# Optimization experiments

Measured on AMD Instinct MI355X. Metric: run time of the kernel, lower is better.

The kernel has to match this reference:

```python
import jax, jax.numpy as jnp
import numpy as np

GRID = 32
N_NODES = GRID * GRID          # 1024
PATCH = 1
C_IN = 3
NODE_F = C_IN * PATCH * PATCH  # 3
HID = 256
N_CLASSES = 10


def _build_norm_adj():
    # 5-point grid stencil + self loops, symmetrically normalized: D^-1/2 A D^-1/2
    adj = np.zeros((N_NODES, N_NODES), dtype=np.float32)
    idx = np.arange(N_NODES)
    i, j = idx // GRID, idx % GRID
    adj[idx, idx] = 1.0
    for di, dj in [(-1, 0), (1, 0), (0, -1), (0, 1)]:
        ni, nj = i + di, j + dj
        ok = (ni >= 0) & (ni < GRID) & (nj >= 0) & (nj < GRID)
        adj[idx[ok], (ni * GRID + nj)[ok]] = 1.0
    deg = adj.sum(axis=1)
    dis = np.where(deg > 0, deg ** -0.5, 0.0).astype(np.float32)
    return jnp.asarray(dis[:, None] * adj * dis[None, :])


def _image_to_graph(x):
    # [B,C,H,W] -> [B, grid, patch, grid, patch] blocks -> [B, N, C*patch^2]
    B = x.shape[0]
    x = x.reshape(B, C_IN, GRID, PATCH, GRID, PATCH)
    x = jnp.transpose(x, (0, 2, 4, 1, 3, 5))
    return x.reshape(B, N_NODES, NODE_F)


def setup_inputs() -> dict:
    key = jax.random.key(0)
    ks = jax.random.split(key, 10)
    s = 0.05
    return {
        "x": jax.random.normal(ks[0], (256, 3, 32, 32), dtype=jnp.float32),
        "W1": jax.random.normal(ks[1], (HID, NODE_F), dtype=jnp.float32) * s,
        "b1": jnp.zeros((HID,), dtype=jnp.float32),
        "W2": jax.random.normal(ks[2], (HID, HID), dtype=jnp.float32) * s,
        "b2": jnp.zeros((HID,), dtype=jnp.float32),
        "W3": jax.random.normal(ks[3], (HID // 2, HID), dtype=jnp.float32) * s,
        "b3": jnp.zeros((HID // 2,), dtype=jnp.float32),
        "Wc": jax.random.normal(ks[4], (N_CLASSES, N_NODES * (HID // 2)), dtype=jnp.float32) * s,
        "bc": jnp.zeros((N_CLASSES,), dtype=jnp.float32),
        "adj": _build_norm_adj(),
    }


def _gc(h, W, b, adj):
    # Linear, then fixed-adjacency aggregation, then ReLU
    h = jnp.einsum('bnf,hf->bnh', h, W) + b
    h = jnp.einsum('mn,bnh->bmh', adj, h)
    return jax.nn.relu(h)


def reference(x, W1, b1, W2, b2, W3, b3, Wc, bc, adj):
    h = _image_to_graph(x)                 # [B, N, 3]
    h = _gc(h, W1, b1, adj)                # [B, N, 256]
    h = _gc(h, W2, b2, adj)                # [B, N, 256]
    h = _gc(h, W3, b3, adj)                # [B, N, 128]
    h = h.reshape(h.shape[0], -1)          # [B, N*128]
    return h @ Wc.T + bc                   # [B, 10]
```

## Files before the change

### kernel.cpp

```cpp
#include <hip/hip_runtime.h>
#include <stdint.h>

#define N_NODES 1024
#define NCLS 10
#define KDIM 131072

typedef unsigned short u16;
typedef __bf16 bf16x8 __attribute__((ext_vector_type(8)));
typedef float f32x4 __attribute__((ext_vector_type(4)));
typedef float f32x2 __attribute__((ext_vector_type(2)));

__device__ __forceinline__ float b2f_lo(uint32_t u) {
  union { float f; uint32_t u; } v; v.u = u << 16; return v.f;
}
__device__ __forceinline__ float b2f_hi(uint32_t u) {
  union { float f; uint32_t u; } v; v.u = u & 0xFFFF0000u; return v.f;
}
__device__ __forceinline__ u16 f2b(float f) {
  union { float f; uint32_t u; } v; v.f = f;
  uint32_t r = v.u + 0x7FFF + ((v.u >> 16) & 1);
  return (u16)(r >> 16);
}
__device__ __forceinline__ uint32_t pkbf(float a, float b) {
#if __has_builtin(__builtin_amdgcn_cvt_pk_bf16_f32)
  typedef __bf16 bf2 __attribute__((ext_vector_type(2)));
  bf2 r = __builtin_amdgcn_cvt_pk_bf16_f32(a, b);
  union { bf2 v; uint32_t u; } c; c.v = r; return c.u;
#else
  union { float f; uint32_t u; } va, vb; va.f = a; vb.f = b;
  uint32_t ra = (va.u + 0x7FFF + ((va.u >> 16) & 1)) >> 16;
  uint32_t rb = (vb.u + 0x7FFF + ((vb.u >> 16) & 1)) & 0xFFFF0000u;
  return ra | rb;
#endif
}
__device__ __forceinline__ uint32_t pkbf2(f32x2 z) { return pkbf(z.x, z.y); }

__device__ __forceinline__ void async_copy16(const u16* g, u16* l) {
  __builtin_amdgcn_global_load_lds(
      (const __attribute__((address_space(1))) void*)g,
      (__attribute__((address_space(3))) void*)l, 16, 0, 0);
}

__device__ __forceinline__ void agg8p(uint4 v, float c, f32x2* acc) {
  const uint32_t* u = (const uint32_t*)&v;
  f32x2 cv = {c, c};
#pragma unroll
  for (int e = 0; e < 4; e++) {
    f32x2 p = {b2f_lo(u[e]), b2f_hi(u[e])};
    acc[e] += p * cv;
  }
}

__global__ __launch_bounds__(256) void prep_wfrag_kernel(const float* __restrict__ w,
                                                         u16* __restrict__ o, int n) {
  int i = blockIdx.x * 256 + threadIdx.x;
  if (i >= n) return;
  int j = i & 7;
  int l = (i >> 3) & 63;
  int kq = (i >> 9) & 7;
  int nt = i >> 12;
  o[i] = f2b(w[(nt * 16 + (l & 15)) * 256 + kq * 32 + (l >> 4) * 8 + j]);
}

__global__ __launch_bounds__(256) void prep_wc_kernel(const float* __restrict__ wc,
                                                      u16* __restrict__ o) {
  int i = blockIdx.x * 256 + threadIdx.x;
  int row = i >> 17;
  int col = i & (KDIM - 1);
  o[i] = (row < NCLS) ? f2b(wc[row * KDIM + col]) : (u16)0;
}

__global__ __launch_bounds__(256) void prep_tab_kernel(const float* __restrict__ adj,
                                                       int* __restrict__ nbi,
                                                       float* __restrict__ nbc,
                                                       float* __restrict__ r) {
  int m = blockIdx.x * 256 + threadIdx.x;
  if (m >= N_NODES) return;
  int i = m >> 5, j = m & 31;
  const float* arow = adj + (size_t)m * N_NODES;
  int n[5]; float c[5];
  n[0] = m;                      c[0] = arow[m];
  n[1] = (i > 0)  ? m - 32 : m;  c[1] = (i > 0)  ? arow[m - 32] : 0.f;
  n[2] = (i < 31) ? m + 32 : m;  c[2] = (i < 31) ? arow[m + 32] : 0.f;
  n[3] = (j > 0)  ? m - 1  : m;  c[3] = (j > 0)  ? arow[m - 1]  : 0.f;
  n[4] = (j < 31) ? m + 1  : m;  c[4] = (j < 31) ? arow[m + 1]  : 0.f;
  float s = 0.f;
#pragma unroll
  for (int t = 0; t < 5; t++) { nbi[m * 5 + t] = n[t]; nbc[m * 5 + t] = c[t]; s += c[t]; }
  r[m] = s;
}

__global__ __launch_bounds__(256) void outinit_kernel(const float* __restrict__ bc,
                                                      float* __restrict__ out) {
  int idx = blockIdx.x * 256 + threadIdx.x;
  if (idx < 256 * NCLS) out[idx] = bc[idx % NCLS];
}

__global__ __launch_bounds__(256) void l1agg_kernel(
    const float* __restrict__ x,
    const float* __restrict__ W1,
    const float* __restrict__ b1,
    const int* __restrict__ nbi, const float* __restrict__ nbc,
    const float* __restrict__ r,
    u16* __restrict__ g)
{
  __shared__ u16 h1s[128 * 256];
  __shared__ float gxs[128][4];
  __shared__ float W1s[768];
  __shared__ float b1s[256];
  int p0 = blockIdx.x * 64;
  int b = p0 >> 10;
  int m0 = p0 & 1023;
  int e0 = m0 - 32;
  int tid = threadIdx.x;

  b1s[tid] = b1[tid];
  for (int i = tid; i < 768; i += 256) W1s[i] = W1[i];

  if (tid < 128) {
    int n = e0 + tid;
    float g0 = 0.f, g1 = 0.f, g2 = 0.f, rn = 0.f;
    if (n >= 0 && n < N_NODES) {
      const float* xb = x + (size_t)b * 3072;
#pragma unroll
      for (int t = 0; t < 5; t++) {
        int nb = nbi[n * 5 + t]; float cf = nbc[n * 5 + t];
        g0 += cf * xb[nb];
        g1 += cf * xb[1024 + nb];
        g2 += cf * xb[2048 + nb];
      }
      rn = r[n];
    }
    gxs[tid][0] = g0; gxs[tid][1] = g1; gxs[tid][2] = g2; gxs[tid][3] = rn;
  }
  __syncthreads();

  int ch8 = (tid & 31) * 8;
  f32x2 wp[3][4], bp[4];
#pragma unroll
  for (int p = 0; p < 4; p++) {
    int c = ch8 + 2 * p;
    wp[0][p] = (f32x2){W1s[c * 3],     W1s[(c + 1) * 3]};
    wp[1][p] = (f32x2){W1s[c * 3 + 1], W1s[(c + 1) * 3 + 1]};
    wp[2][p] = (f32x2){W1s[c * 3 + 2], W1s[(c + 1) * 3 + 2]};
    bp[p]    = (f32x2){b1s[c],         b1s[c + 1]};
  }

#pragma unroll
  for (int it = 0; it < 16; it++) {
    int node = (tid >> 5) + it * 8;
    f32x2 g0v = {gxs[node][0], gxs[node][0]};
    f32x2 g1v = {gxs[node][1], gxs[node][1]};
    f32x2 g2v = {gxs[node][2], gxs[node][2]};
    f32x2 rnv = {gxs[node][3], gxs[node][3]};
    uint32_t pk[4];
#pragma unroll
    for (int p = 0; p < 4; p++) {
      f32x2 z = g0v * wp[0][p] + g1v * wp[1][p] + g2v * wp[2][p] + rnv * bp[p];
      z.x = fmaxf(z.x, 0.f); z.y = fmaxf(z.y, 0.f);
      pk[p] = pkbf2(z);
    }
    *(uint4*)&h1s[node * 256 + ch8] = *(uint4*)pk;
  }
  __syncthreads();

#pragma unroll
  for (int it = 0; it < 8; it++) {
    int node = (tid >> 5) + it * 8;
    int m = m0 + node;
    f32x2 acc[4] = {};
#pragma unroll
    for (int t = 0; t < 5; t++) {
      int nb = nbi[m * 5 + t]; float cf = nbc[m * 5 + t];
      agg8p(*(const uint4*)&h1s[(nb - e0) * 256 + ch8], cf, acc);
    }
    uint4 o;
    o.x = pkbf2(acc[0]); o.y = pkbf2(acc[1]);
    o.z = pkbf2(acc[2]); o.w = pkbf2(acc[3]);
    *(uint4*)&g[(size_t)(p0 + node) * 256 + ch8] = o;
  }
}

__global__ __launch_bounds__(256) void mm_kernel(
    const u16* __restrict__ A, const u16* __restrict__ Wf,
    const float* __restrict__ bias, const float* __restrict__ r,
    u16* __restrict__ C, int N)
{
  const int K = 256;
  __shared__ u16 As[2][128 * 64];
  int n0 = blockIdx.x * 128;
  int m0 = blockIdx.y * 128;
  int tid = threadIdx.x;
  int w = tid >> 6, l = tid & 63;
  int wm = w >> 1, wn = w & 1;

  int r8 = l >> 3, oct = l & 7;
  int so = (oct ^ r8) << 3;
  const u16* ga0 = A + (size_t)(m0 + w * 32 + r8) * K + so;

#define MM_ISSUE(kq, buf) \
  _Pragma("unroll") for (int q = 0; q < 4; q++) \
    async_copy16(ga0 + (size_t)q * 8 * K + (kq) * 64, &As[buf][(w * 32 + q * 8) * 64]);

  MM_ISSUE(0, 0);

  f32x4 acc[4][4] = {};
  int lrow = l & 15, lq = l >> 4;
  int s = lrow & 7;
  const u16* wfb = Wf + (((size_t)(n0 >> 4) + wn * 4) * 8) * 512 + l * 8;

#pragma unroll
  for (int kq = 0; kq < 4; kq++) {
    int buf = kq & 1;
    __syncthreads();
    if (kq < 3) { MM_ISSUE(kq + 1, buf ^ 1); }
    const u16* pa = &As[buf][(wm * 64 + lrow) * 64];
#pragma unroll
    for (int kh = 0; kh < 2; kh++) {
      int kk = kq * 2 + kh;
      int po = (((kh << 2) | lq) ^ s) << 3;
      bf16x8 af[4], bf[4];
#pragma unroll
      for (int t = 0; t < 4; t++) {
        af[t] = *(const bf16x8*)(pa + t * 16 * 64 + po);
        bf[t] = *(const bf16x8*)(wfb + ((size_t)t * 8 + kk) * 512);
      }
#pragma unroll
      for (int mt = 0; mt < 4; mt++)
#pragma unroll
        for (int nt = 0; nt < 4; nt++)
          acc[mt][nt] = __builtin_amdgcn_mfma_f32_16x16x32_bf16(af[mt], bf[nt], acc[mt][nt], 0, 0, 0);
    }
  }
#undef MM_ISSUE

#pragma unroll
  for (int mt = 0; mt < 4; mt++)
#pragma unroll
    for (int nt = 0; nt < 4; nt++) {
      f32x4 v = acc[mt][nt];
      int col = n0 + wn * 64 + nt * 16 + lrow;
      float bs = bias[col];
#pragma unroll
      for (int i2 = 0; i2 < 4; i2++) {
        int row = m0 + wm * 64 + mt * 16 + lq * 4 + i2;
        float val = v[i2] + r[row & 1023] * bs;
        C[(size_t)row * N + col] = f2b(fmaxf(val, 0.f));
      }
    }
}

__global__ __launch_bounds__(256) void mm3agg_kernel(
    const u16* __restrict__ H,
    const u16* __restrict__ W3f,
    const float* __restrict__ bias, const float* __restrict__ r,
    const int* __restrict__ nbi, const float* __restrict__ nbc,
    u16* __restrict__ C)
{
  const int AST = 40;
  __shared__ u16 As[2][128 * AST];
  int m0 = blockIdx.x * 128;
  int tid = threadIdx.x;
  int w = tid >> 6, l = tid & 63;
  int wm = w >> 1, wn = w & 1;

  int arow = tid >> 1;
  int acol = (tid & 1) * 16;
  int pg = m0 + arow;
  int node0 = pg & 1023;
  const u16* hb = H + ((size_t)(pg >> 10) << 10) * 256 + acol;
  const u16* nbp[5]; float cf[5];
#pragma unroll
  for (int j = 0; j < 5; j++) {
    nbp[j] = hb + (size_t)nbi[node0 * 5 + j] * 256;
    cf[j] = nbc[node0 * 5 + j];
  }

#define M3_LOADA(kq) \
  _Pragma("unroll") for (int j = 0; j < 5; j++) \
    _Pragma("unroll") for (int q = 0; q < 2; q++) \
      L[j][q] = *(const uint4*)(nbp[j] + (kq) * 32 + q * 8);

#define M3_AGGSTORE(buf) { \
  u16* dst = &As[buf][arow * AST + acol]; \
  _Pragma("unroll") for (int q = 0; q < 2; q++) { \
    f32x2 a2[4] = {}; \
    _Pragma("unroll") for (int j = 0; j < 5; j++) agg8p(L[j][q], cf[j], a2); \
    uint4 o; \
    o.x = pkbf2(a2[0]); o.y = pkbf2(a2[1]); \
    o.z = pkbf2(a2[2]); o.w = pkbf2(a2[3]); \
    *(uint4*)(dst + q * 8) = o; \
  } }

  uint4 L[5][2];
  M3_LOADA(0);
  M3_AGGSTORE(0);

  f32x4 acc[4][4] = {};
  int lrow = l & 15, lq = l >> 4;
  const u16* wfb = W3f + ((size_t)wn * 4 * 8) * 512 + l * 8;

#pragma unroll
  for (int kq = 0; kq < 8; kq++) {
    int buf = kq & 1;
    __syncthreads();
    if (kq < 7) M3_LOADA(kq + 1);
    const u16* pa = &As[buf][(wm * 64 + lrow) * AST + lq * 8];
    bf16x8 af[4], bf[4];
#pragma unroll
    for (int t = 0; t < 4; t++) {
      af[t] = *(const bf16x8*)(pa + t * 16 * AST);
      bf[t] = *(const bf16x8*)(wfb + ((size_t)t * 8 + kq) * 512);
    }
#pragma unroll
    for (int mt = 0; mt < 4; mt++)
#pragma unroll
      for (int nt = 0; nt < 4; nt++)
        acc[mt][nt] = __builtin_amdgcn_mfma_f32_16x16x32_bf16(af[mt], bf[nt], acc[mt][nt], 0, 0, 0);
    if (kq < 7) M3_AGGSTORE(buf ^ 1);
  }
#undef M3_LOADA
#undef M3_AGGSTORE

#pragma unroll
  for (int mt = 0; mt < 4; mt++)
#pragma unroll
    for (int nt = 0; nt < 4; nt++) {
      f32x4 v = acc[mt][nt];
      int col = wn * 64 + nt * 16 + lrow;
      float bs = bias[col];
#pragma unroll
      for (int i2 = 0; i2 < 4; i2++) {
        int row = m0 + wm * 64 + mt * 16 + lq * 4 + i2;
        float val = v[i2] + r[row & 1023] * bs;
        C[(size_t)row * 128 + col] = f2b(fmaxf(val, 0.f));
      }
    }
}

__global__ __launch_bounds__(256) void cls_kernel(
    const u16* __restrict__ h3,
    const u16* __restrict__ Wcb,
    float* __restrict__ out,
    int b0)
{
  int mt = blockIdx.x;
  int split = blockIdx.y;
  int w = threadIdx.x >> 6, l = threadIdx.x & 63;
  int lrow = l & 15, lq = l >> 4;
  f32x4 acc = {};
  int kbase = split * 4096 + w * 1024;
  const u16* pa = h3 + (size_t)(mt * 16 + lrow) * KDIM + kbase + lq * 8;
  const u16* pb = Wcb + (size_t)lrow * KDIM + kbase + lq * 8;
#pragma unroll 4
  for (int kk = 0; kk < 1024; kk += 32) {
    bf16x8 a = *(const bf16x8*)(pa + kk);
    bf16x8 b = *(const bf16x8*)(pb + kk);
    acc = __builtin_amdgcn_mfma_f32_16x16x32_bf16(a, b, acc, 0, 0, 0);
  }
  if (lrow < NCLS) {
#pragma unroll
    for (int i2 = 0; i2 < 4; i2++) {
      int b = b0 + mt * 16 + lq * 4 + i2;
      atomicAdd(&out[b * NCLS + lrow], acc[i2]);
    }
  }
}

extern "C" void kernel_launch(void* const* d_in, const int* in_sizes, int n_in,
                              void* d_out, int out_size, void* d_ws, size_t ws_size,
                              hipStream_t stream) {
  const float* x   = (const float*)d_in[0];
  const float* W1  = (const float*)d_in[1];
  const float* b1  = (const float*)d_in[2];
  const float* W2  = (const float*)d_in[3];
  const float* b2  = (const float*)d_in[4];
  const float* W3  = (const float*)d_in[5];
  const float* b3  = (const float*)d_in[6];
  const float* Wc  = (const float*)d_in[7];
  const float* bc  = (const float*)d_in[8];
  const float* adj = (const float*)d_in[9];
  float* out = (float*)d_out;
  const int B = 256;

  uint8_t* ws = (uint8_t*)d_ws;
  u16* W2f = (u16*)ws;  ws += (size_t)256 * 256 * 2;
  u16* W3f = (u16*)ws;  ws += (size_t)128 * 256 * 2;
  u16* Wcb = (u16*)ws;  ws += (size_t)16 * KDIM * 2;
  float* rr  = (float*)ws; ws += 1024 * 4;
  int*   nbi = (int*)ws;   ws += 1024 * 5 * 4;
  float* nbc = (float*)ws; ws += 1024 * 5 * 4;
  uintptr_t al = ((uintptr_t)ws + 255) & ~(uintptr_t)255;
  ws = (uint8_t*)al;
  size_t used = (size_t)(ws - (uint8_t*)d_ws);
  size_t avail = (ws_size > used) ? ws_size - used : 0;
  int chunk = 256;
  while (chunk > 32 && (size_t)chunk * 1024 * 256 * 2 * 2 > avail) chunk >>= 1;
  u16* bufA = (u16*)ws;
  u16* bufB = bufA + (size_t)chunk * 1024 * 256;

  prep_wfrag_kernel<<<256, 256, 0, stream>>>(W2, W2f, 256 * 256);
  prep_wfrag_kernel<<<128, 256, 0, stream>>>(W3, W3f, 128 * 256);
  prep_wc_kernel<<<(16 * KDIM) / 256, 256, 0, stream>>>(Wc, Wcb);
  prep_tab_kernel<<<4, 256, 0, stream>>>(adj, nbi, nbc, rr);
  outinit_kernel<<<(256 * NCLS + 255) / 256, 256, 0, stream>>>(bc, out);

  for (int b0 = 0; b0 < B; b0 += chunk) {
    const float* xb = x + (size_t)b0 * 3 * 1024;
    int M = chunk * 1024;
    l1agg_kernel<<<M / 64, 256, 0, stream>>>(xb, W1, b1, nbi, nbc, rr, bufB);
    {
      dim3 g(2, M / 128);
      mm_kernel<<<g, 256, 0, stream>>>(bufB, W2f, b2, rr, bufA, 256);
    }
    mm3agg_kernel<<<M / 128, 256, 0, stream>>>(bufA, W3f, b3, rr, nbi, nbc, bufB);
    dim3 gc(chunk / 16, 32);
    cls_kernel<<<gc, 256, 0, stream>>>(bufB, Wcb, out, b0);
  }
}
```

Baseline: 372.1 us.

## Reorder layer-3 to matmul-then-aggregate on narrower 128-channel output

Layer 3 previously aggregated the 256-channel input inside the matmul kernel before multiplying by W3. It now runs the generic matmul kernel in raw mode to produce the 128-channel product, then a separate gather kernel aggregates, adds scaled bias and applies ReLU. This halves the channels touched by the neighbour gather and reuses the tuned matmul path. In exchange it adds a kernel launch and a full write/read round trip of the intermediate, and it changes where bf16 rounding occurs.

```diff
diff --git a/kernel.cpp b/kernel.cpp
--- a/kernel.cpp
+++ b/kernel.cpp
@@ -184,7 +184,7 @@
 __global__ __launch_bounds__(256) void mm_kernel(
     const u16* __restrict__ A, const u16* __restrict__ Wf,
     const float* __restrict__ bias, const float* __restrict__ r,
-    u16* __restrict__ C, int N)
+    u16* __restrict__ C, int N, int raw)
 {
   const int K = 256;
   __shared__ u16 As[2][128 * 64];
@@ -244,98 +244,49 @@
 #pragma unroll
       for (int i2 = 0; i2 < 4; i2++) {
         int row = m0 + wm * 64 + mt * 16 + lq * 4 + i2;
-        float val = v[i2] + r[row & 1023] * bs;
-        C[(size_t)row * N + col] = f2b(fmaxf(val, 0.f));
+        float val;
+        if (raw) val = v[i2];
+        else     val = fmaxf(v[i2] + r[row & 1023] * bs, 0.f);
+        C[(size_t)row * N + col] = f2b(val);
       }
     }
 }
 
-__global__ __launch_bounds__(256) void mm3agg_kernel(
-    const u16* __restrict__ H,
-    const u16* __restrict__ W3f,
-    const float* __restrict__ bias, const float* __restrict__ r,
+__global__ __launch_bounds__(256) void aggz_kernel(
+    const u16* __restrict__ Z,
+    const float* __restrict__ b3,
+    const float* __restrict__ r,
     const int* __restrict__ nbi, const float* __restrict__ nbc,
-    u16* __restrict__ C)
+    u16* __restrict__ h3)
 {
-  const int AST = 40;
-  __shared__ u16 As[2][128 * AST];
-  int m0 = blockIdx.x * 128;
-  int tid = threadIdx.x;
-  int w = tid >> 6, l = tid & 63;
-  int wm = w >> 1, wn = w & 1;
-
-  int arow = tid >> 1;
-  int acol = (tid & 1) * 16;
-  int pg = m0 + arow;
-  int node0 = pg & 1023;
-  const u16* hb = H + ((size_t)(pg >> 10) << 10) * 256 + acol;
-  const u16* nbp[5]; float cf[5];
-#pragma unroll
-  for (int j = 0; j < 5; j++) {
-    nbp[j] = hb + (size_t)nbi[node0 * 5 + j] * 256;
-    cf[j] = nbc[node0 * 5 + j];
-  }
-
-#define M3_LOADA(kq) \
-  _Pragma("unroll") for (int j = 0; j < 5; j++) \
-    _Pragma("unroll") for (int q = 0; q < 2; q++) \
-      L[j][q] = *(const uint4*)(nbp[j] + (kq) * 32 + q * 8);
-
-#define M3_AGGSTORE(buf) { \
-  u16* dst = &As[buf][arow * AST + acol]; \
-  _Pragma("unroll") for (int q = 0; q < 2; q++) { \
-    f32x2 a2[4] = {}; \
-    _Pragma("unroll") for (int j = 0; j < 5; j++) agg8p(L[j][q], cf[j], a2); \
-    uint4 o; \
-    o.x = pkbf2(a2[0]); o.y = pkbf2(a2[1]); \
-    o.z = pkbf2(a2[2]); o.w = pkbf2(a2[3]); \
-    *(uint4*)(dst + q * 8) = o; \
-  } }
-
-  uint4 L[5][2];
-  M3_LOADA(0);
-  M3_AGGSTORE(0);
-
-  f32x4 acc[4][4] = {};
-  int lrow = l & 15, lq = l >> 4;
-  const u16* wfb = W3f + ((size_t)wn * 4 * 8) * 512 + l * 8;
-
-#pragma unroll
-  for (int kq = 0; kq < 8; kq++) {
-    int buf = kq & 1;
-    __syncthreads();
-    if (kq < 7) M3_LOADA(kq + 1);
-    const u16* pa = &As[buf][(wm * 64 + lrow) * AST + lq * 8];
-    bf16x8 af[4], bf[4];
-#pragma unroll
-    for (int t = 0; t < 4; t++) {
-      af[t] = *(const bf16x8*)(pa + t * 16 * AST);
-      bf[t] = *(const bf16x8*)(wfb + ((size_t)t * 8 + kq) * 512);
-    }
-#pragma unroll
-    for (int mt = 0; mt < 4; mt++)
-#pragma unroll
-      for (int nt = 0; nt < 4; nt++)
-        acc[mt][nt] = __builtin_amdgcn_mfma_f32_16x16x32_bf16(af[mt], bf[nt], acc[mt][nt], 0, 0, 0);
-    if (kq < 7) M3_AGGSTORE(buf ^ 1);
-  }
-#undef M3_LOADA
-#undef M3_AGGSTORE
-
-#pragma unroll
-  for (int mt = 0; mt < 4; mt++)
-#pragma unroll
-    for (int nt = 0; nt < 4; nt++) {
-      f32x4 v = acc[mt][nt];
-      int col = wn * 64 + nt * 16 + lrow;
-      float bs = bias[col];
-#pragma unroll
-      for (int i2 = 0; i2 < 4; i2++) {
-        int row = m0 + wm * 64 + mt * 16 + lq * 4 + i2;
-        float val = v[i2] + r[row & 1023] * bs;
-        C[(size_t)row * 128 + col] = f2b(fmaxf(val, 0.f));
-      }
-    }
+  int p = (blockIdx.x * 256 + threadIdx.x) >> 4;
+  int l16 = threadIdx.x & 15;
+  int b = p >> 10, m = p & 1023;
+  const u16* zb = Z + ((size_t)b << 10) * 128;
+  int col = l16 * 8;
+  f32x2 acc[4] = {};
+#pragma unroll
+  for (int t = 0; t < 5; t++) {
+    int nb = nbi[m * 5 + t]; float cf = nbc[m * 5 + t];
+    agg8p(*(const uint4*)(zb + (size_t)nb * 128 + col), cf, acc);
+  }
+  float rn = r[m];
+  float4 bA = *(const float4*)(b3 + col);
+  float4 bB = *(const float4*)(b3 + col + 4);
+  f32x2 rv = {rn, rn};
+  acc[0] += rv * (f32x2){bA.x, bA.y};
+  acc[1] += rv * (f32x2){bA.z, bA.w};
+  acc[2] += rv * (f32x2){bB.x, bB.y};
+  acc[3] += rv * (f32x2){bB.z, bB.w};
+#pragma unroll
+  for (int e = 0; e < 4; e++) {
+    acc[e].x = fmaxf(acc[e].x, 0.f);
+    acc[e].y = fmaxf(acc[e].y, 0.f);
+  }
+  uint4 o;
+  o.x = pkbf2(acc[0]); o.y = pkbf2(acc[1]);
+  o.z = pkbf2(acc[2]); o.w = pkbf2(acc[3]);
+  *(uint4*)(h3 + (size_t)p * 128 + col) = o;
 }
 
 __global__ __launch_bounds__(256) void cls_kernel(
@@ -411,10 +362,14 @@
     l1agg_kernel<<<M / 64, 256, 0, stream>>>(xb, W1, b1, nbi, nbc, rr, bufB);
     {
       dim3 g(2, M / 128);
-      mm_kernel<<<g, 256, 0, stream>>>(bufB, W2f, b2, rr, bufA, 256);
-    }
-    mm3agg_kernel<<<M / 128, 256, 0, stream>>>(bufA, W3f, b3, rr, nbi, nbc, bufB);
+      mm_kernel<<<g, 256, 0, stream>>>(bufB, W2f, b2, rr, bufA, 256, 0);
+    }
+    {
+      dim3 g(1, M / 128);
+      mm_kernel<<<g, 256, 0, stream>>>(bufA, W3f, b3, rr, bufB, 128, 1);
+    }
+    aggz_kernel<<<M / 16, 256, 0, stream>>>(bufB, b3, rr, nbi, nbc, bufA);
     dim3 gc(chunk / 16, 32);
-    cls_kernel<<<gc, 256, 0, stream>>>(bufB, Wcb, out, b0);
-  }
-}
+    cls_kernel<<<gc, 256, 0, stream>>>(bufA, Wcb, out, b0);
+  }
+}
```

Result: slower. 393.5 us (+5.8%).
